# Performance work log

Hardware: AMD Instinct MI355X
Metric: run time of the kernel (lower is better)

Reference implementation:

```python
import jax, jax.numpy as jnp
import numpy as np

B, S, HID = 2, 2048, 2048
NH, NKV, D = 16, 4, 128
N_REP = NH // NKV
SCALING = D ** -0.5
QMAX = 7  # int4 symmetric: 2**(4-1)-1
NEG_INF = -1e9


def rotate_half(x):
    x1, x2 = x[..., : x.shape[-1] // 2], x[..., x.shape[-1] // 2 :]
    return jnp.concatenate((-x2, x1), axis=-1)


def apply_rope(q, k, cos, sin):
    # cos/sin: [B,S,D] -> [B,1,S,D] (unsqueeze_dim=1)
    cos, sin = cos[:, None], sin[:, None]
    return q * cos + rotate_half(q) * sin, k * cos + rotate_half(k) * sin


def quantize_int4_per_head(x):
    # x: [B,H,S,D]; per-head 0.995 quantile of |x| -> symmetric int4.
    Bx, H, Sx, Dx = x.shape
    per_head = jnp.abs(x).transpose(1, 0, 2, 3).reshape(H, -1)  # [H, B*S*D]
    abs_max = jnp.quantile(per_head, 0.995, axis=1)             # [H]
    scale = jnp.maximum(abs_max, 1e-6) / QMAX                    # [H]
    scale4 = scale.reshape(1, H, 1, 1)
    q = jnp.clip(jnp.round(x / scale4), -QMAX, QMAX).astype(jnp.int8)
    return q, scale4


def setup_inputs() -> dict:
    key = jax.random.key(0)
    ks = jax.random.split(key, 6)
    hidden_states = jax.random.normal(ks[0], (B, S, HID), dtype=jnp.float32)
    Wq = jax.random.normal(ks[1], (HID, NH * D), dtype=jnp.float32) * 0.02
    Wk = jax.random.normal(ks[2], (HID, NKV * D), dtype=jnp.float32) * 0.02
    Wv = jax.random.normal(ks[3], (HID, NKV * D), dtype=jnp.float32) * 0.02
    Wo = jax.random.normal(ks[4], (NH * D, HID), dtype=jnp.float32) * 0.02
    # Rotary embeddings (theta=10000)
    inv_freq = 1.0 / (10000.0 ** (jnp.arange(0, D, 2, dtype=jnp.float32) / D))
    freqs = jnp.arange(S, dtype=jnp.float32)[:, None] * inv_freq[None, :]  # [S, D/2]
    emb = jnp.concatenate([freqs, freqs], axis=-1)                          # [S, D]
    cos = jnp.broadcast_to(jnp.cos(emb)[None], (B, S, D)).astype(jnp.float32)
    sin = jnp.broadcast_to(jnp.sin(emb)[None], (B, S, D)).astype(jnp.float32)
    # Causal additive mask [1,1,S,S]
    causal = jnp.tril(jnp.ones((S, S), dtype=bool))
    attention_mask = jnp.where(causal, 0.0, NEG_INF)[None, None].astype(jnp.float32)
    return {
        "hidden_states": hidden_states, "cos": cos, "sin": sin,
        "attention_mask": attention_mask,
        "Wq": Wq, "Wk": Wk, "Wv": Wv, "Wo": Wo,
    }


def reference(hidden_states, cos, sin, attention_mask, Wq, Wk, Wv, Wo):
    # Projections -> [B, H, S, D]
    q = (hidden_states @ Wq).reshape(B, S, NH, D).transpose(0, 2, 1, 3)
    k = (hidden_states @ Wk).reshape(B, S, NKV, D).transpose(0, 2, 1, 3)
    v = (hidden_states @ Wv).reshape(B, S, NKV, D).transpose(0, 2, 1, 3)
    q, k = apply_rope(q, k, cos, sin)
    # GQA: repeat_interleave kv heads to NH
    k_rep = jnp.repeat(k, N_REP, axis=1)
    v_rep = jnp.repeat(v, N_REP, axis=1)
    # int4 per-head quantization side path (detached in original)
    q_int8, q_scale = quantize_int4_per_head(q)
    k_int8, k_scale = quantize_int4_per_head(k_rep)
    # Attention in full precision (as in the original eager path)
    scores = jnp.einsum("bhqd,bhkd->bhqk", q, k_rep) * SCALING
    scores = scores + attention_mask[:, :, :, :S]
    attn = jax.nn.softmax(scores, axis=-1)
    ctx = jnp.einsum("bhqk,bhkd->bhqd", attn, v_rep)
    out = ctx.transpose(0, 2, 1, 3).reshape(B, S, NH * D) @ Wo
    return out, q_int8, q_scale, k_int8, k_scale
```

## Files before the change

kernel.cpp:

```cpp
#include <hip/hip_runtime.h>
#include <math.h>

#define SCALING_ 0.08838834764831845f
#define SM_C     0.12751741f

typedef __bf16 bf16;
typedef bf16 bf16x8 __attribute__((ext_vector_type(8)));
typedef bf16 bf16x4 __attribute__((ext_vector_type(4)));
typedef float f32x4 __attribute__((ext_vector_type(4)));

__global__ __launch_bounds__(256) void sgemm_qkv(
    const float* __restrict__ A, const float* __restrict__ Wq,
    const float* __restrict__ Wk, const float* __restrict__ Wv,
    float* __restrict__ qbuf, float* __restrict__ kfb, float* __restrict__ vfb)
{
    __shared__ __align__(16) float As[16][132];
    __shared__ __align__(16) float Bs[16][132];
    const int tid = threadIdx.x;
    const int tx = tid & 15, ty = tid >> 4;
    const int bx = blockIdx.x, by = blockIdx.y;

    const float* W; float* Cc; int N, hh, nh;
    if (bx < 16)      { W = Wq; Cc = qbuf; N = 2048; hh = bx;      nh = 16; }
    else if (bx < 20) { W = Wk; Cc = kfb;  N = 512;  hh = bx - 16; nh = 4;  }
    else              { W = Wv; Cc = vfb;  N = 512;  hh = bx - 20; nh = 4;  }
    const int row0 = by * 128;
    const int col0 = hh * 128;

    float acc[8][8];
    #pragma unroll
    for (int i = 0; i < 8; i++)
        #pragma unroll
        for (int j = 0; j < 8; j++) acc[i][j] = 0.f;

    const int ar = tid >> 1, ac8 = (tid & 1) * 8;
    const int bk = tid >> 5, bn4 = (tid & 31) * 4;
    const float* Aptr = A + (row0 + ar) * 2048 + ac8;
    const float* Bptr = W + bk * N + col0 + bn4;

    float4 a0 = *(const float4*)(Aptr);
    float4 a1 = *(const float4*)(Aptr + 4);
    float4 b0 = *(const float4*)(Bptr);
    float4 b1 = *(const float4*)(Bptr + 8 * N);

    for (int k0 = 0; k0 < 2048; k0 += 16) {
        __syncthreads();
        As[ac8 + 0][ar] = a0.x; As[ac8 + 1][ar] = a0.y;
        As[ac8 + 2][ar] = a0.z; As[ac8 + 3][ar] = a0.w;
        As[ac8 + 4][ar] = a1.x; As[ac8 + 5][ar] = a1.y;
        As[ac8 + 6][ar] = a1.z; As[ac8 + 7][ar] = a1.w;
        *(float4*)&Bs[bk][bn4]     = b0;
        *(float4*)&Bs[bk + 8][bn4] = b1;
        __syncthreads();
        if (k0 + 16 < 2048) {
            a0 = *(const float4*)(Aptr + k0 + 16);
            a1 = *(const float4*)(Aptr + k0 + 20);
            b0 = *(const float4*)(Bptr + (long)(k0 + 16) * N);
            b1 = *(const float4*)(Bptr + (long)(k0 + 24) * N);
        }
        #pragma unroll
        for (int kk = 0; kk < 16; kk++) {
            const float4 av0 = *(const float4*)&As[kk][ty * 8];
            const float4 av1 = *(const float4*)&As[kk][ty * 8 + 4];
            const float4 bv0 = *(const float4*)&Bs[kk][tx * 4];
            const float4 bv1 = *(const float4*)&Bs[kk][64 + tx * 4];
            const float a[8] = {av0.x,av0.y,av0.z,av0.w,av1.x,av1.y,av1.z,av1.w};
            const float b[8] = {bv0.x,bv0.y,bv0.z,bv0.w,bv1.x,bv1.y,bv1.z,bv1.w};
            #pragma unroll
            for (int i = 0; i < 8; i++)
                #pragma unroll
                for (int j = 0; j < 8; j++) acc[i][j] += a[i] * b[j];
        }
    }

    #pragma unroll
    for (int i = 0; i < 8; i++) {
        const int r = row0 + ty * 8 + i;
        const int bb = r >> 11, s = r & 2047;
        float* rowp = Cc + ((long)((bb * nh + hh) * 2048 + s)) * 128;
        float4 v0 = {acc[i][0], acc[i][1], acc[i][2], acc[i][3]};
        float4 v1 = {acc[i][4], acc[i][5], acc[i][6], acc[i][7]};
        *(float4*)(rowp + tx * 4)      = v0;
        *(float4*)(rowp + 64 + tx * 4) = v1;
    }
}

__global__ __launch_bounds__(256) void rope_cvt_k(
    float* __restrict__ buf, bf16* __restrict__ outb,
    const float* __restrict__ cosb, const float* __restrict__ sinb, int nheads)
{
    const int t = blockIdx.x * 256 + threadIdx.x;
    const int d = t & 63;
    const int s = (t >> 6) & 2047;
    const int bh = t >> 17;
    const int base = (bh * 2048 + s) * 128;
    const int b = (nheads == 16) ? (bh >> 4) : (bh >> 2);
    const int cbase = (b * 2048 + s) * 128;
    const float x1 = buf[base + d], x2 = buf[base + d + 64];
    const float c1 = cosb[cbase + d],      s1 = sinb[cbase + d];
    const float c2 = cosb[cbase + d + 64], s2 = sinb[cbase + d + 64];
    const float y1 = x1 * c1 - x2 * s1;
    const float y2 = x2 * c2 + x1 * s2;
    buf[base + d]       = y1;
    buf[base + d + 64]  = y2;
    outb[base + d]      = (bf16)y1;
    outb[base + d + 64] = (bf16)y2;
}

__global__ __launch_bounds__(256) void transpose_v(
    const float* __restrict__ V, bf16* __restrict__ Vt)
{
    __shared__ float t[32][33];
    const int s0 = blockIdx.x * 32, d0 = blockIdx.y * 32;
    const long base = (long)blockIdx.z * 262144;
    const int r = threadIdx.x >> 3, c4 = (threadIdx.x & 7) * 4;
    const float4 v = *(const float4*)(V + base + (s0 + r) * 128 + d0 + c4);
    t[r][c4] = v.x; t[r][c4+1] = v.y; t[r][c4+2] = v.z; t[r][c4+3] = v.w;
    __syncthreads();
    bf16x4 o = { (bf16)t[c4][r], (bf16)t[c4+1][r], (bf16)t[c4+2][r], (bf16)t[c4+3][r] };
    *(bf16x4*)(Vt + base + (d0 + r) * 2048 + s0 + c4) = o;
}

__global__ __launch_bounds__(256) void transpose_wo(
    const float* __restrict__ W, bf16* __restrict__ Wt)
{
    __shared__ float t[32][33];
    const int n0 = blockIdx.x * 32, k0 = blockIdx.y * 32;
    const int r = threadIdx.x >> 3, c4 = (threadIdx.x & 7) * 4;
    const float4 v = *(const float4*)(W + (k0 + r) * 2048 + n0 + c4);
    t[r][c4] = v.x; t[r][c4+1] = v.y; t[r][c4+2] = v.z; t[r][c4+3] = v.w;
    __syncthreads();
    bf16x4 o = { (bf16)t[c4][r], (bf16)t[c4+1][r], (bf16)t[c4+2][r], (bf16)t[c4+3][r] };
    *(bf16x4*)(Wt + (n0 + r) * 2048 + k0 + c4) = o;
}

__global__ __launch_bounds__(256) void attn_mfma(
    const bf16* __restrict__ qb, const bf16* __restrict__ kb,
    const bf16* __restrict__ vt, bf16* __restrict__ ctx)
{
    __shared__ bf16 Qs[64][136];
    __shared__ bf16 Ks[64][136];
    __shared__ bf16 Vt[128][72];
    __shared__ bf16 Ps[64][72];

    const int tid = threadIdx.x;
    const int lane = tid & 63, wave = tid >> 6;
    const int l16 = lane & 15, quad = lane >> 4;
    const int qt = 31 - blockIdx.x;
    const int h = blockIdx.y, b = blockIdx.z;
    const int q0 = qt * 64;
    const int wrow = wave * 16;

    const bf16* qbase = qb + ((long)((b * 16 + h) * 2048 + q0)) * 128;
    const bf16* kbase = kb + ((long)((b * 4 + (h >> 2)) * 2048)) * 128;
    const bf16* vbase = vt + ((long)((b * 4 + (h >> 2)) * 128)) * 2048;

    #pragma unroll
    for (int it = 0; it < 4; it++) {
        const int f = it * 256 + tid;
        const int r = f >> 4, c8 = (f & 15) * 8;
        *(bf16x8*)&Qs[r][c8] = *(const bf16x8*)(qbase + r * 128 + c8);
    }
    __syncthreads();
    bf16x8 aQ[4];
    #pragma unroll
    for (int ks = 0; ks < 4; ks++)
        aQ[ks] = *(const bf16x8*)&Qs[wrow + l16][ks * 32 + quad * 8];

    float m_i[4] = {-INFINITY, -INFINITY, -INFINITY, -INFINITY};
    float l_i[4] = {0.f, 0.f, 0.f, 0.f};
    f32x4 O[8];
    #pragma unroll
    for (int n = 0; n < 8; n++) O[n] = (f32x4){0.f, 0.f, 0.f, 0.f};

    for (int kt = 0; kt <= qt; kt++) {
        const int kt0 = kt * 64;
        __syncthreads();
        #pragma unroll
        for (int it = 0; it < 4; it++) {
            const int f = it * 256 + tid;
            const int r = f >> 4, c8 = (f & 15) * 8;
            *(bf16x8*)&Ks[r][c8] = *(const bf16x8*)(kbase + (kt0 + r) * 128 + c8);
        }
        #pragma unroll
        for (int it = 0; it < 8; it++) {
            const int f = it * 256 + tid;
            const int d = f >> 4, k4 = (f & 15) * 4;
            *(bf16x4*)&Vt[d][k4] = *(const bf16x4*)(vbase + d * 2048 + kt0 + k4);
        }
        __syncthreads();

        f32x4 S[4];
        #pragma unroll
        for (int nt = 0; nt < 4; nt++) S[nt] = (f32x4){0.f, 0.f, 0.f, 0.f};
        #pragma unroll
        for (int nt = 0; nt < 4; nt++) {
            #pragma unroll
            for (int ks = 0; ks < 4; ks++) {
                const bf16x8 bK = *(const bf16x8*)&Ks[nt * 16 + l16][ks * 32 + quad * 8];
                S[nt] = __builtin_amdgcn_mfma_f32_16x16x32_bf16(aQ[ks], bK, S[nt], 0, 0, 0);
            }
        }

        const bool diag = (kt == qt);
        #pragma unroll
        for (int i = 0; i < 4; i++) {
            const int qr = q0 + wrow + quad * 4 + i;
            float sv[4];
            #pragma unroll
            for (int nt = 0; nt < 4; nt++) {
                float x = S[nt][i];
                if (diag && (kt0 + nt * 16 + l16 > qr)) x = -1e30f;
                sv[nt] = x;
            }
            float rm = fmaxf(fmaxf(sv[0], sv[1]), fmaxf(sv[2], sv[3]));
            rm = fmaxf(rm, __shfl_xor(rm, 1));
            rm = fmaxf(rm, __shfl_xor(rm, 2));
            rm = fmaxf(rm, __shfl_xor(rm, 4));
            rm = fmaxf(rm, __shfl_xor(rm, 8));
            const float mn = fmaxf(m_i[i], rm);
            const float alpha = exp2f((m_i[i] - mn) * SM_C);
            m_i[i] = mn;
            float rs = 0.f;
            #pragma unroll
            for (int nt = 0; nt < 4; nt++) {
                const float p = exp2f((sv[nt] - mn) * SM_C);
                rs += p;
                Ps[wrow + quad * 4 + i][nt * 16 + l16] = (bf16)p;
            }
            rs += __shfl_xor(rs, 1);
            rs += __shfl_xor(rs, 2);
            rs += __shfl_xor(rs, 4);
            rs += __shfl_xor(rs, 8);
            l_i[i] = l_i[i] * alpha + rs;
            #pragma unroll
            for (int n = 0; n < 8; n++) O[n][i] *= alpha;
        }

        bf16x8 aP[2];
        aP[0] = *(const bf16x8*)&Ps[wrow + l16][quad * 8];
        aP[1] = *(const bf16x8*)&Ps[wrow + l16][32 + quad * 8];
        #pragma unroll
        for (int nt = 0; nt < 8; nt++) {
            #pragma unroll
            for (int ks = 0; ks < 2; ks++) {
                const bf16x8 bV = *(const bf16x8*)&Vt[nt * 16 + l16][ks * 32 + quad * 8];
                O[nt] = __builtin_amdgcn_mfma_f32_16x16x32_bf16(aP[ks], bV, O[nt], 0, 0, 0);
            }
        }
    }

    #pragma unroll
    for (int i = 0; i < 4; i++) {
        const float inv = 1.f / l_i[i];
        const int s = q0 + wrow + quad * 4 + i;
        bf16* dst = ctx + ((long)(b * 2048 + s)) * 2048 + h * 128;
        #pragma unroll
        for (int nt = 0; nt < 8; nt++)
            dst[nt * 16 + l16] = (bf16)(O[nt][i] * inv);
    }
}

__global__ __launch_bounds__(256) void gemm_o_mfma(
    const bf16* __restrict__ A, const bf16* __restrict__ Bt,
    float* __restrict__ C)
{
    __shared__ bf16 As[128][40];
    __shared__ bf16 Bs[128][40];
    const int tid = threadIdx.x;
    const int lane = tid & 63, wave = tid >> 6;
    const int l16 = lane & 15, quad = lane >> 4;
    const int m0 = blockIdx.y * 128, n0 = blockIdx.x * 128;
    const int wm = (wave >> 1) * 64, wn = (wave & 1) * 64;

    f32x4 acc[4][4];
    #pragma unroll
    for (int i = 0; i < 4; i++)
        #pragma unroll
        for (int j = 0; j < 4; j++) acc[i][j] = (f32x4){0.f, 0.f, 0.f, 0.f};

    for (int k0 = 0; k0 < 2048; k0 += 32) {
        __syncthreads();
        #pragma unroll
        for (int it = 0; it < 2; it++) {
            const int f = it * 256 + tid;
            const int r = f >> 2, c8 = (f & 3) * 8;
            *(bf16x8*)&As[r][c8] = *(const bf16x8*)(A + (long)(m0 + r) * 2048 + k0 + c8);
            *(bf16x8*)&Bs[r][c8] = *(const bf16x8*)(Bt + (long)(n0 + r) * 2048 + k0 + c8);
        }
        __syncthreads();
        bf16x8 af[4], bf_[4];
        #pragma unroll
        for (int mt = 0; mt < 4; mt++)
            af[mt] = *(const bf16x8*)&As[wm + mt * 16 + l16][quad * 8];
        #pragma unroll
        for (int nt = 0; nt < 4; nt++)
            bf_[nt] = *(const bf16x8*)&Bs[wn + nt * 16 + l16][quad * 8];
        #pragma unroll
        for (int mt = 0; mt < 4; mt++)
            #pragma unroll
            for (int nt = 0; nt < 4; nt++)
                acc[mt][nt] = __builtin_amdgcn_mfma_f32_16x16x32_bf16(af[mt], bf_[nt], acc[mt][nt], 0, 0, 0);
    }

    #pragma unroll
    for (int mt = 0; mt < 4; mt++) {
        #pragma unroll
        for (int r = 0; r < 4; r++) {
            const int row = m0 + wm + mt * 16 + quad * 4 + r;
            float* dst = C + (long)row * 2048 + n0 + wn;
            #pragma unroll
            for (int nt = 0; nt < 4; nt++)
                dst[nt * 16 + l16] = acc[mt][nt][r];
        }
    }
}

__global__ void quant_init(int* __restrict__ qP, int* __restrict__ qC)
{
    const int t = threadIdx.x;
    if (t < 40) { qP[t] = 0; qC[t] = 0; }
}

__global__ __launch_bounds__(256) void hist_zero(int* __restrict__ hist)
{
    hist[blockIdx.x * 256 + threadIdx.x] = 0;
}

__global__ __launch_bounds__(256) void hist_build(
    const float* __restrict__ qbuf, const float* __restrict__ kfb,
    const int* __restrict__ qP, int* __restrict__ hist, int level)
{
    __shared__ int lh[4096];
    const int tid = threadIdx.x;
    const int job = blockIdx.x >> 5, sub = blockIdx.x & 31;
    for (int i = tid; i < 4096; i += 256) lh[i] = 0;
    __syncthreads();
    const int head = job >> 1;
    const int pref = qP[job];
    for (int it = 0; it < 64; it++) {
        const int e = sub * 16384 + it * 256 + tid;
        const int bb = e >> 18, off = e & 262143;
        float v;
        if (head < 16) v = qbuf[(bb * 16 + head) * 262144 + off];
        else           v = kfb[(bb * 4 + (head - 16)) * 262144 + off];
        const unsigned u = __float_as_uint(fabsf(v));
        int bin = -1;
        if (level == 0)      bin = (int)(u >> 20);
        else if (level == 1) { if ((int)(u >> 20) == pref) bin = (int)((u >> 8) & 4095u); }
        else                 { if ((int)(u >> 8)  == pref) bin = (int)(u & 255u); }
        if (bin >= 0) atomicAdd(&lh[bin], 1);
    }
    __syncthreads();
    for (int i = tid; i < 4096; i += 256) {
        const int c = lh[i];
        if (c) atomicAdd(&hist[job * 4096 + i], c);
    }
}

__global__ __launch_bounds__(256) void hist_scan(
    int* __restrict__ qP, int* __restrict__ qC,
    const int* __restrict__ hist, int level)
{
    __shared__ int psum[256];
    __shared__ int sel[2];
    const int job = blockIdx.x, tid = threadIdx.x;
    const int target = (job & 1) ? 521666 : 521665;
    const int t = target - qC[job];
    int loc[16]; int s = 0;
    const int* hb = hist + job * 4096 + tid * 16;
    #pragma unroll
    for (int i = 0; i < 16; i++) { loc[i] = hb[i]; s += loc[i]; }
    psum[tid] = s;
    __syncthreads();
    if (tid == 0) {
        int cum = 0, pick = 255, pcum = 0; bool fnd = false;
        for (int i = 0; i < 256; i++) {
            const int c = psum[i];
            if (!fnd && cum + c > t) { pick = i; pcum = cum; fnd = true; }
            cum += c;
        }
        if (!fnd) pcum = cum - psum[255];
        sel[0] = pick; sel[1] = pcum;
    }
    __syncthreads();
    if (tid == sel[0]) {
        int c = sel[1];
        int bin = 15;
        #pragma unroll
        for (int i = 0; i < 16; i++) {
            if (c + loc[i] > t) { bin = i; break; }
            c += loc[i];
        }
        const int gbin = tid * 16 + bin;
        int p = qP[job];
        if (level == 0)      p = gbin;
        else if (level == 1) p = (p << 12) | gbin;
        else                 p = (p << 8) | gbin;
        qP[job] = p;
        qC[job] = qC[job] + c;
    }
}

__global__ void finalize_scales(const int* __restrict__ qP,
                                float* __restrict__ q_scale, float* __restrict__ k_scale)
{
    const int tid = threadIdx.x;
    const double pos = 0.995 * 524287.0;
    const float fr = (float)(pos - floor(pos));
    if (tid < 16) {
        const float v0 = __uint_as_float((unsigned)qP[2 * tid]);
        const float v1 = __uint_as_float((unsigned)qP[2 * tid + 1]);
        const float am = v0 + fr * (v1 - v0);
        q_scale[tid] = fmaxf(am, 1e-6f) / 7.0f;
    } else if (tid < 32) {
        const int h = tid - 16;
        const int job = (16 + (h >> 2)) * 2;
        const float v0 = __uint_as_float((unsigned)qP[job]);
        const float v1 = __uint_as_float((unsigned)qP[job + 1]);
        const float am = v0 + fr * (v1 - v0);
        k_scale[h] = fmaxf(am, 1e-6f) / 7.0f;
    }
}

__global__ __launch_bounds__(256) void quant_q(
    float* __restrict__ qbuf, const float* __restrict__ q_scale)
{
    const int i = blockIdx.x * 256 + threadIdx.x;
    const int h = (i >> 18) & 15;
    const float sc = q_scale[h];
    float v = rintf(qbuf[i] / sc);
    v = fminf(fmaxf(v, -7.f), 7.f);
    qbuf[i] = v;
}

__global__ __launch_bounds__(256) void quant_k(
    const float* __restrict__ kfb, float* __restrict__ kout,
    const float* __restrict__ k_scale)
{
    const int i = blockIdx.x * 256 + threadIdx.x;
    const int h = (i >> 18) & 15;
    const int bb = i >> 22;
    const int rest = i & 262143;
    const float v = kfb[(bb * 4 + (h >> 2)) * 262144 + rest];
    const float sc = k_scale[h];
    float qv = rintf(v / sc);
    qv = fminf(fmaxf(qv, -7.f), 7.f);
    kout[i] = qv;
}

extern "C" void kernel_launch(void* const* d_in, const int* in_sizes, int n_in,
                              void* d_out, int out_size, void* d_ws, size_t ws_size,
                              hipStream_t stream)
{
    const float* hs   = (const float*)d_in[0];
    const float* cosb = (const float*)d_in[1];
    const float* sinb = (const float*)d_in[2];
    const float* Wq = (const float*)d_in[4];
    const float* Wk = (const float*)d_in[5];
    const float* Wv = (const float*)d_in[6];
    const float* Wo = (const float*)d_in[7];

    float* out     = (float*)d_out;
    float* qbuf    = out + 8388608;
    float* q_scale = out + 16777216;
    float* kqout   = out + 16777232;
    float* k_scale = out + 25165840;

    bf16* qb16 = (bf16*)kqout;
    bf16* kb16 = qb16 + 8388608;
    bf16* vtb  = kb16 + 2097152;

    float* wsf = (float*)d_ws;
    bf16*  ctx16 = (bf16*)wsf;
    float* kfb   = wsf + 4194304;
    float* vfb   = wsf + 6291456;
    bf16*  woT   = (bf16*)(wsf + 8388608);
    int*   qP    = (int*)(wsf + 10485760);
    int*   qC    = qP + 64;
    int*   hist  = qP + 128;

    sgemm_qkv<<<dim3(24, 32), 256, 0, stream>>>(hs, Wq, Wk, Wv, qbuf, kfb, vfb);
    rope_cvt_k<<<16384, 256, 0, stream>>>(qbuf, qb16, cosb, sinb, 16);
    rope_cvt_k<<<4096, 256, 0, stream>>>(kfb, kb16, cosb, sinb, 4);
    transpose_v<<<dim3(64, 4, 8), 256, 0, stream>>>(vfb, vtb);
    transpose_wo<<<dim3(64, 64), 256, 0, stream>>>(Wo, woT);

    attn_mfma<<<dim3(32, 16, 2), 256, 0, stream>>>(qb16, kb16, vtb, ctx16);
    gemm_o_mfma<<<dim3(16, 32), 256, 0, stream>>>(ctx16, woT, out);

    quant_init<<<1, 64, 0, stream>>>(qP, qC);
    for (int lvl = 0; lvl < 3; lvl++) {
        hist_zero<<<640, 256, 0, stream>>>(hist);
        hist_build<<<1280, 256, 0, stream>>>(qbuf, kfb, qP, hist, lvl);
        hist_scan<<<40, 256, 0, stream>>>(qP, qC, hist, lvl);
    }
    finalize_scales<<<1, 64, 0, stream>>>(qP, q_scale, k_scale);

    quant_q<<<32768, 256, 0, stream>>>(qbuf, q_scale);
    quant_k<<<32768, 256, 0, stream>>>(kfb, kqout, k_scale);
}
```

Baseline: 1.258 ms.

## Move V projection to bf16 MFMA, double-buffer QK sgemm, fuse quant kernels

The V projection moves out of the fp32 SIMT GEMM into a new bf16 MFMA GEMM. It uses a pre-transposed bf16 copy of Wv, and the activations are converted to bf16 on load. The remaining Q/K fp32 GEMM now double-buffers its shared-memory tiles, which needs one barrier per k-step instead of two. The two quantization kernels merge into one launch. V precision drops to bf16, and the extra transpose kernel adds a small fixed cost.

```diff
diff --git a/kernel.cpp b/kernel.cpp
--- a/kernel.cpp
+++ b/kernel.cpp
@@ -9,21 +9,20 @@
 typedef bf16 bf16x4 __attribute__((ext_vector_type(4)));
 typedef float f32x4 __attribute__((ext_vector_type(4)));
 
-__global__ __launch_bounds__(256) void sgemm_qkv(
+__global__ __launch_bounds__(256) void sgemm_qk(
     const float* __restrict__ A, const float* __restrict__ Wq,
-    const float* __restrict__ Wk, const float* __restrict__ Wv,
-    float* __restrict__ qbuf, float* __restrict__ kfb, float* __restrict__ vfb)
-{
-    __shared__ __align__(16) float As[16][132];
-    __shared__ __align__(16) float Bs[16][132];
+    const float* __restrict__ Wk,
+    float* __restrict__ qbuf, float* __restrict__ kfb)
+{
+    __shared__ __align__(16) float As[2][16][132];
+    __shared__ __align__(16) float Bs[2][16][132];
     const int tid = threadIdx.x;
     const int tx = tid & 15, ty = tid >> 4;
     const int bx = blockIdx.x, by = blockIdx.y;
 
     const float* W; float* Cc; int N, hh, nh;
-    if (bx < 16)      { W = Wq; Cc = qbuf; N = 2048; hh = bx;      nh = 16; }
-    else if (bx < 20) { W = Wk; Cc = kfb;  N = 512;  hh = bx - 16; nh = 4;  }
-    else              { W = Wv; Cc = vfb;  N = 512;  hh = bx - 20; nh = 4;  }
+    if (bx < 16) { W = Wq; Cc = qbuf; N = 2048; hh = bx;      nh = 16; }
+    else         { W = Wk; Cc = kfb;  N = 512;  hh = bx - 16; nh = 4;  }
     const int row0 = by * 128;
     const int col0 = hh * 128;
 
@@ -42,17 +41,18 @@
     float4 a1 = *(const float4*)(Aptr + 4);
     float4 b0 = *(const float4*)(Bptr);
     float4 b1 = *(const float4*)(Bptr + 8 * N);
-
+    As[0][ac8 + 0][ar] = a0.x; As[0][ac8 + 1][ar] = a0.y;
+    As[0][ac8 + 2][ar] = a0.z; As[0][ac8 + 3][ar] = a0.w;
+    As[0][ac8 + 4][ar] = a1.x; As[0][ac8 + 5][ar] = a1.y;
+    As[0][ac8 + 6][ar] = a1.z; As[0][ac8 + 7][ar] = a1.w;
+    *(float4*)&Bs[0][bk][bn4]     = b0;
+    *(float4*)&Bs[0][bk + 8][bn4] = b1;
+    __syncthreads();
+
+    int cur = 0;
     for (int k0 = 0; k0 < 2048; k0 += 16) {
-        __syncthreads();
-        As[ac8 + 0][ar] = a0.x; As[ac8 + 1][ar] = a0.y;
-        As[ac8 + 2][ar] = a0.z; As[ac8 + 3][ar] = a0.w;
-        As[ac8 + 4][ar] = a1.x; As[ac8 + 5][ar] = a1.y;
-        As[ac8 + 6][ar] = a1.z; As[ac8 + 7][ar] = a1.w;
-        *(float4*)&Bs[bk][bn4]     = b0;
-        *(float4*)&Bs[bk + 8][bn4] = b1;
-        __syncthreads();
-        if (k0 + 16 < 2048) {
+        const bool more = (k0 + 16) < 2048;
+        if (more) {
             a0 = *(const float4*)(Aptr + k0 + 16);
             a1 = *(const float4*)(Aptr + k0 + 20);
             b0 = *(const float4*)(Bptr + (long)(k0 + 16) * N);
@@ -60,16 +60,27 @@
         }
         #pragma unroll
         for (int kk = 0; kk < 16; kk++) {
-            const float4 av0 = *(const float4*)&As[kk][ty * 8];
-            const float4 av1 = *(const float4*)&As[kk][ty * 8 + 4];
-            const float4 bv0 = *(const float4*)&Bs[kk][tx * 4];
-            const float4 bv1 = *(const float4*)&Bs[kk][64 + tx * 4];
+            const float4 av0 = *(const float4*)&As[cur][kk][ty * 8];
+            const float4 av1 = *(const float4*)&As[cur][kk][ty * 8 + 4];
+            const float4 bv0 = *(const float4*)&Bs[cur][kk][tx * 4];
+            const float4 bv1 = *(const float4*)&Bs[cur][kk][64 + tx * 4];
             const float a[8] = {av0.x,av0.y,av0.z,av0.w,av1.x,av1.y,av1.z,av1.w};
             const float b[8] = {bv0.x,bv0.y,bv0.z,bv0.w,bv1.x,bv1.y,bv1.z,bv1.w};
             #pragma unroll
             for (int i = 0; i < 8; i++)
                 #pragma unroll
                 for (int j = 0; j < 8; j++) acc[i][j] += a[i] * b[j];
+        }
+        if (more) {
+            const int nx = cur ^ 1;
+            As[nx][ac8 + 0][ar] = a0.x; As[nx][ac8 + 1][ar] = a0.y;
+            As[nx][ac8 + 2][ar] = a0.z; As[nx][ac8 + 3][ar] = a0.w;
+            As[nx][ac8 + 4][ar] = a1.x; As[nx][ac8 + 5][ar] = a1.y;
+            As[nx][ac8 + 6][ar] = a1.z; As[nx][ac8 + 7][ar] = a1.w;
+            *(float4*)&Bs[nx][bk][bn4]     = b0;
+            *(float4*)&Bs[nx][bk + 8][bn4] = b1;
+            __syncthreads();
+            cur = nx;
         }
     }
 
@@ -82,6 +93,80 @@
         float4 v1 = {acc[i][4], acc[i][5], acc[i][6], acc[i][7]};
         *(float4*)(rowp + tx * 4)      = v0;
         *(float4*)(rowp + 64 + tx * 4) = v1;
+    }
+}
+
+__global__ __launch_bounds__(256) void transpose_wv(
+    const float* __restrict__ W, bf16* __restrict__ Wt)
+{
+    __shared__ float t[32][33];
+    const int n0 = blockIdx.x * 32, k0 = blockIdx.y * 32;
+    const int r = threadIdx.x >> 3, c4 = (threadIdx.x & 7) * 4;
+    const float4 v = *(const float4*)(W + (long)(k0 + r) * 512 + n0 + c4);
+    t[r][c4] = v.x; t[r][c4+1] = v.y; t[r][c4+2] = v.z; t[r][c4+3] = v.w;
+    __syncthreads();
+    bf16x4 o = { (bf16)t[c4][r], (bf16)t[c4+1][r], (bf16)t[c4+2][r], (bf16)t[c4+3][r] };
+    *(bf16x4*)(Wt + (long)(n0 + r) * 2048 + k0 + c4) = o;
+}
+
+__global__ __launch_bounds__(256) void gemm_v_mfma(
+    const float* __restrict__ A, const bf16* __restrict__ Bt,
+    float* __restrict__ vfb)
+{
+    __shared__ bf16 As[128][40];
+    __shared__ bf16 Bs[128][40];
+    const int tid = threadIdx.x;
+    const int lane = tid & 63, wave = tid >> 6;
+    const int l16 = lane & 15, quad = lane >> 4;
+    const int m0 = blockIdx.y * 128, n0 = blockIdx.x * 128;
+    const int hh = blockIdx.x;
+    const int wm = (wave >> 1) * 64, wn = (wave & 1) * 64;
+
+    f32x4 acc[4][4];
+    #pragma unroll
+    for (int i = 0; i < 4; i++)
+        #pragma unroll
+        for (int j = 0; j < 4; j++) acc[i][j] = (f32x4){0.f, 0.f, 0.f, 0.f};
+
+    for (int k0 = 0; k0 < 2048; k0 += 32) {
+        __syncthreads();
+        #pragma unroll
+        for (int it = 0; it < 2; it++) {
+            const int f = it * 256 + tid;
+            const int r = f >> 2, c8 = (f & 3) * 8;
+            const float4 x0 = *(const float4*)(A + (long)(m0 + r) * 2048 + k0 + c8);
+            const float4 x1 = *(const float4*)(A + (long)(m0 + r) * 2048 + k0 + c8 + 4);
+            bf16x8 ab = { (bf16)x0.x, (bf16)x0.y, (bf16)x0.z, (bf16)x0.w,
+                          (bf16)x1.x, (bf16)x1.y, (bf16)x1.z, (bf16)x1.w };
+            *(bf16x8*)&As[r][c8] = ab;
+            *(bf16x8*)&Bs[r][c8] = *(const bf16x8*)(Bt + (long)(n0 + r) * 2048 + k0 + c8);
+        }
+        __syncthreads();
+        bf16x8 af[4], bf_[4];
+        #pragma unroll
+        for (int mt = 0; mt < 4; mt++)
+            af[mt] = *(const bf16x8*)&As[wm + mt * 16 + l16][quad * 8];
+        #pragma unroll
+        for (int nt = 0; nt < 4; nt++)
+            bf_[nt] = *(const bf16x8*)&Bs[wn + nt * 16 + l16][quad * 8];
+        #pragma unroll
+        for (int mt = 0; mt < 4; mt++)
+            #pragma unroll
+            for (int nt = 0; nt < 4; nt++)
+                acc[mt][nt] = __builtin_amdgcn_mfma_f32_16x16x32_bf16(af[mt], bf_[nt], acc[mt][nt], 0, 0, 0);
+    }
+
+    #pragma unroll
+    for (int mt = 0; mt < 4; mt++) {
+        #pragma unroll
+        for (int rr = 0; rr < 4; rr++) {
+            const int r = m0 + wm + mt * 16 + quad * 4 + rr;
+            const int bb = r >> 11, s = r & 2047;
+            float* dst = vfb + ((long)((bb * 4 + hh) * 2048 + s)) * 128 + wn;
+            #pragma unroll
+            for (int nt = 0; nt < 4; nt++)
+                dst[nt * 16 + l16] = acc[mt][nt][rr];
+        }
     }
 }
 
@@ -423,30 +508,27 @@
     }
 }
 
-__global__ __launch_bounds__(256) void quant_q(
-    float* __restrict__ qbuf, const float* __restrict__ q_scale)
+__global__ __launch_bounds__(256) void quant_qk(
+    float* __restrict__ qbuf, const float* __restrict__ kfb,
+    float* __restrict__ kout,
+    const float* __restrict__ q_scale, const float* __restrict__ k_scale)
 {
     const int i = blockIdx.x * 256 + threadIdx.x;
-    const int h = (i >> 18) & 15;
-    const float sc = q_scale[h];
-    float v = rintf(qbuf[i] / sc);
-    v = fminf(fmaxf(v, -7.f), 7.f);
-    qbuf[i] = v;
-}
-
-__global__ __launch_bounds__(256) void quant_k(
-    const float* __restrict__ kfb, float* __restrict__ kout,
-    const float* __restrict__ k_scale)
-{
-    const int i = blockIdx.x * 256 + threadIdx.x;
-    const int h = (i >> 18) & 15;
-    const int bb = i >> 22;
-    const int rest = i & 262143;
-    const float v = kfb[(bb * 4 + (h >> 2)) * 262144 + rest];
-    const float sc = k_scale[h];
-    float qv = rintf(v / sc);
-    qv = fminf(fmaxf(qv, -7.f), 7.f);
-    kout[i] = qv;
+    if (i < 8388608) {
+        const int h = (i >> 18) & 15;
+        const float sc = q_scale[h];
+        float v = rintf(qbuf[i] / sc);
+        qbuf[i] = fminf(fmaxf(v, -7.f), 7.f);
+    } else {
+        const int j = i - 8388608;
+        const int h = (j >> 18) & 15;
+        const int bb = j >> 22;
+        const int rest = j & 262143;
+        const float v = kfb[(bb * 4 + (h >> 2)) * 262144 + rest];
+        const float sc = k_scale[h];
+        float qv = rintf(v / sc);
+        kout[j] = fminf(fmaxf(qv, -7.f), 7.f);
+    }
 }
 
 extern "C" void kernel_launch(void* const* d_in, const int* in_sizes, int n_in,
@@ -479,8 +561,12 @@
     int*   qP    = (int*)(wsf + 10485760);
     int*   qC    = qP + 64;
     int*   hist  = qP + 128;
-
-    sgemm_qkv<<<dim3(24, 32), 256, 0, stream>>>(hs, Wq, Wk, Wv, qbuf, kfb, vfb);
+    bf16*  wvT   = (bf16*)(wsf + 10649728);
+
+    transpose_wv<<<dim3(16, 64), 256, 0, stream>>>(Wv, wvT);
+    sgemm_qk<<<dim3(20, 32), 256, 0, stream>>>(hs, Wq, Wk, qbuf, kfb);
+    gemm_v_mfma<<<dim3(4, 32), 256, 0, stream>>>(hs, wvT, vfb);
+
     rope_cvt_k<<<16384, 256, 0, stream>>>(qbuf, qb16, cosb, sinb, 16);
     rope_cvt_k<<<4096, 256, 0, stream>>>(kfb, kb16, cosb, sinb, 4);
     transpose_v<<<dim3(64, 4, 8), 256, 0, stream>>>(vfb, vtb);
@@ -497,6 +583,5 @@
     }
     finalize_scales<<<1, 64, 0, stream>>>(qP, q_scale, k_scale);
 
-    quant_q<<<32768, 256, 0, stream>>>(qbuf, q_scale);
-    quant_k<<<32768, 256, 0, stream>>>(kfb, kqout, k_scale);
-}
+    quant_qk<<<65536, 256, 0, stream>>>(qbuf, kfb, kqout, q_scale, k_scale);
+}
```

New measurement: 1.305 ms. +3.8%, slower.
